# Performance work log

Hardware: AMD Instinct MI355X
Metric: run time of the kernel (lower is better)

The kernel has to match this reference:

```python
import jax, jax.numpy as jnp
import numpy as np

B, C, D = 512, 50000, 256
N_LOADED = 40000


def setup_inputs() -> dict:
    key = jax.random.key(0)
    k1, k2, k3, k4 = jax.random.split(key, 4)
    visual_feats = jax.random.normal(k1, (B, D), dtype=jnp.float32)
    text_feats = jax.random.normal(k2, (C, D), dtype=jnp.float32)
    # sparse multi-hot labels; force class 0 positive for every row so the
    # positive set (intersected with loaded ids) is never empty
    batch_label = (jax.random.uniform(k3, (B, C)) < 0.02).astype(jnp.int32)
    batch_label = batch_label.at[:, 0].set(1)
    # distinct loaded class ids; force id 0 to be loaded
    ids = jax.random.permutation(k4, C)[:N_LOADED].astype(jnp.int32)
    ids = jnp.sort(ids).at[0].set(0)
    return {
        "visual_feats": visual_feats,
        "text_feats": text_feats,
        "batch_label": batch_label,
        "class_ids_loaded": ids,
        "d_space": D,
    }


def reference(visual_feats, text_feats, batch_label, class_ids_loaded, d_space):
    num_classes = text_feats.shape[0]
    # membership mask for loaded class ids (the set() intersection in torch)
    loaded = jnp.zeros((num_classes,), dtype=bool).at[class_ids_loaded].set(True)

    # cosine similarity; note: torch adds 1e-6 eps only to text-feature norms
    v = visual_feats / jnp.linalg.norm(visual_feats, axis=1, keepdims=True)
    t = text_feats / (1e-6 + jnp.linalg.norm(text_feats, axis=1, keepdims=True))
    S = v @ t.T  # [B, C]

    pos = (batch_label != 0) & loaded[None, :]  # ragged positive sets, as mask
    neg = (batch_label == 0) & loaded[None, :]  # ragged negative sets, as mask

    # denominator: sum of exp(sim) over negatives, per row
    denom = jnp.sum(jnp.where(neg, jnp.exp(S), 0.0), axis=1)  # [B]
    n_pos = jnp.sum(pos, axis=1).astype(S.dtype)  # [B]

    # per-row loss: mean over positives of -log(exp(s_p)/denom) = log(denom)-s_p
    per_row = jnp.sum(jnp.where(pos, jnp.log(denom)[:, None] - S, 0.0), axis=1) / n_pos
    return jnp.mean(per_row).reshape(1)
```

## Files before the change

kernel.cpp:

```cpp
#include <hip/hip_runtime.h>
#include <math.h>

#define D_DIM 256
#define TM 128
#define TN 128
#define BK 32
#define NBP 392
#define CBPR 7
#define CBLKS (CBPR * 512)

typedef __attribute__((ext_vector_type(8))) short short8;
typedef __attribute__((ext_vector_type(4))) float floatx4;
typedef unsigned long long u64;

__device__ __forceinline__ unsigned short f2bf(float f) {
    unsigned int u = __float_as_uint(f);
    u += 0x7FFFu + ((u >> 16) & 1u);
    return (unsigned short)(u >> 16);
}

__device__ __forceinline__ void gload16(const void* g, void* lds) {
    __builtin_amdgcn_global_load_lds(
        (const __attribute__((address_space(1))) unsigned int*)g,
        (__attribute__((address_space(3))) unsigned int*)lds, 16, 0, 0);
}

__global__ __launch_bounds__(256) void prep_compress(
    const float* __restrict__ V, const float* __restrict__ T,
    const int* __restrict__ label, const int* __restrict__ ids,
    u64* __restrict__ loadedmask, u64* __restrict__ posmask,
    unsigned short* __restrict__ Vb, unsigned short* __restrict__ Tb,
    float* __restrict__ gaccum, unsigned int* __restrict__ gcount,
    int B, int C, int n_loaded, int WPR) {
    const int bid = blockIdx.x;
    const int tid = threadIdx.x;
    const int lane = tid & 63;

    if (bid < CBLKS) {
        int row = bid / CBPR;
        int sub = bid - row * CBPR;
        int wl  = tid >> 6;
        int w0col = (sub * 4 + wl) * 2048;
        if (w0col >= C) return;
        const int* lp = label + (size_t)row * C;
        int4 lo[4], hi[4];
        #pragma unroll
        for (int r = 0; r < 4; ++r) {
            int c0 = w0col + r * 512 + lane * 8;
            if (c0 < C) {
                lo[r] = *(const int4*)(lp + c0);
                hi[r] = *(const int4*)(lp + c0 + 4);
            } else {
                lo[r] = make_int4(0, 0, 0, 0);
                hi[r] = make_int4(0, 0, 0, 0);
            }
        }
        #pragma unroll
        for (int r = 0; r < 4; ++r) {
            unsigned int by =
                (lo[r].x ? 1u : 0u) | (lo[r].y ? 2u : 0u) |
                (lo[r].z ? 4u : 0u) | (lo[r].w ? 8u : 0u) |
                (hi[r].x ? 16u : 0u) | (hi[r].y ? 32u : 0u) |
                (hi[r].z ? 64u : 0u) | (hi[r].w ? 128u : 0u);
            u64 wv = (u64)by << (8 * (lane & 7));
            wv |= __shfl_xor(wv, 1);
            wv |= __shfl_xor(wv, 2);
            wv |= __shfl_xor(wv, 4);
            if ((lane & 7) == 0) {
                int wc = ((w0col + r * 512) >> 6) + (lane >> 3);
                if (wc < WPR) posmask[(size_t)row * WPR + wc] = wv;
            }
        }
        return;
    }

    int ptid = (bid - CBLKS) * 256 + tid;
    if (ptid == 0) { *gcount = 0u; *gaccum = 0.f; }
    if (ptid < WPR) {
        int base = ptid << 6;
        int lo = 0, hi = n_loaded;
        while (lo < hi) { int mid = (lo + hi) >> 1; if (ids[mid] < base) lo = mid + 1; else hi = mid; }
        u64 m = 0;
        for (int i = lo; i < n_loaded; ++i) {
            int v = ids[i]; if (v >= base + 64) break;
            m |= 1ull << (v - base);
        }
        loadedmask[ptid] = m;
    }
    int wave = ptid >> 6;
    if (wave >= B + C) return;
    bool isV = wave < B;
    const float* src = isV ? (V + (size_t)wave * D_DIM)
                           : (T + (size_t)(wave - B) * D_DIM);
    float4 x = ((const float4*)src)[lane];
    float ss = x.x * x.x + x.y * x.y + x.z * x.z + x.w * x.w;
    #pragma unroll
    for (int off = 32; off > 0; off >>= 1) ss += __shfl_xor(ss, off);
    float nrm = sqrtf(ss);
    float s = isV ? (1.0f / nrm) : (1.0f / (1e-6f + nrm));
    ushort4 o;
    o.x = f2bf(x.x * s); o.y = f2bf(x.y * s);
    o.z = f2bf(x.z * s); o.w = f2bf(x.w * s);
    unsigned short* dst = isV ? (Vb + (size_t)wave * D_DIM)
                              : (Tb + (size_t)(wave - B) * D_DIM);
    ((ushort4*)dst)[lane] = o;
}

__global__ __launch_bounds__(256) void gemm_fused(
    const unsigned short* __restrict__ Vb, const unsigned short* __restrict__ Tb,
    const u64* __restrict__ posmask, const u64* __restrict__ loadedmask,
    float* __restrict__ denomP, float* __restrict__ posP, int C, int WPR) {
    __shared__ unsigned short As[TM * BK];
    __shared__ unsigned short Bs[TN * BK];
    __shared__ float sDen[TM], sPos[TM];

    const int tid  = threadIdx.x;
    const int lane = tid & 63;
    const int w    = tid >> 6;
    const int m0 = blockIdx.x * TM;
    const int n0 = blockIdx.y * TN;

    if (tid < TM) { sDen[tid] = 0.f; sPos[tid] = 0.f; }

    const int sra = lane >> 2;
    const int kc  = (lane & 3) * 8;
    int ga  = m0 + w * 32 + sra;
    int gb0 = n0 + w * 32 + sra;
    int gb1 = gb0 + 16;
    if (gb0 >= C) gb0 = C - 1;
    if (gb1 >= C) gb1 = C - 1;
    const unsigned short* gA0 = Vb + (size_t)ga * D_DIM + kc;
    const unsigned short* gA1 = gA0 + (size_t)16 * D_DIM;
    const unsigned short* gB0 = Tb + (size_t)gb0 * D_DIM + kc;
    const unsigned short* gB1 = Tb + (size_t)gb1 * D_DIM + kc;
    unsigned short* lA0 = &As[w * 32 * BK];
    unsigned short* lA1 = lA0 + 16 * BK;
    unsigned short* lB0 = &Bs[w * 32 * BK];
    unsigned short* lB1 = lB0 + 16 * BK;

    const int wm = (w >> 1) * 64;
    const int wn = (w & 1) * 64;
    const int fr = lane & 15;
    const int quad = lane >> 4;

    floatx4 acc[4][4];
    #pragma unroll
    for (int mi = 0; mi < 4; mi++)
        #pragma unroll
        for (int ni = 0; ni < 4; ni++) acc[mi][ni] = (floatx4)0.f;

    #pragma unroll
    for (int kt = 0; kt < D_DIM / BK; ++kt) {
        if (kt) __syncthreads();
        const int kb = kt * BK;
        gload16(gA0 + kb, lA0);
        gload16(gA1 + kb, lA1);
        gload16(gB0 + kb, lB0);
        gload16(gB1 + kb, lB1);
        __syncthreads();
        short8 af[4], bf[4];
        #pragma unroll
        for (int mi = 0; mi < 4; mi++)
            af[mi] = *(const short8*)&As[(wm + mi * 16 + fr) * BK + quad * 8];
        #pragma unroll
        for (int ni = 0; ni < 4; ni++)
            bf[ni] = *(const short8*)&Bs[(wn + ni * 16 + fr) * BK + quad * 8];
        #pragma unroll
        for (int mi = 0; mi < 4; mi++)
            #pragma unroll
            for (int ni = 0; ni < 4; ni++)
                acc[mi][ni] = __builtin_amdgcn_mfma_f32_16x16x32_bf16(
                    af[mi], bf[ni], acc[mi][ni], 0, 0, 0);
    }

    const int wcol = (n0 + wn) >> 6;
    const u64 loadedw = loadedmask[wcol];
    #pragma unroll
    for (int mi = 0; mi < 4; mi++) {
        #pragma unroll
        for (int i = 0; i < 4; i++) {
            const int mloc = wm + mi * 16 + quad * 4 + i;
            const u64 praw = posmask[(size_t)(m0 + mloc) * WPR + wcol];
            const u64 posw = praw & loadedw;
            const u64 negw = loadedw & ~praw;
            float den = 0.f, pos = 0.f;
            #pragma unroll
            for (int ni = 0; ni < 4; ni++) {
                const float s = acc[mi][ni][i];
                const int bit = ni * 16 + fr;
                if ((negw >> bit) & 1) den += __expf(s);
                if ((posw >> bit) & 1) pos += s;
            }
            #pragma unroll
            for (int off = 8; off >= 1; off >>= 1) {
                den += __shfl_xor(den, off);
                pos += __shfl_xor(pos, off);
            }
            if (fr == 0) {
                if (den != 0.f) atomicAdd(&sDen[mloc], den);
                if (pos != 0.f) atomicAdd(&sPos[mloc], pos);
            }
        }
    }
    __syncthreads();
    if (tid < TM) {
        denomP[(size_t)(m0 + tid) * NBP + blockIdx.y] = sDen[tid];
        posP[(size_t)(m0 + tid) * NBP + blockIdx.y]   = sPos[tid];
    }
}

__global__ void reduce_rows(const float* __restrict__ denomP, const float* __restrict__ posP,
                            const u64* __restrict__ posmask, const u64* __restrict__ loadedmask,
                            float* __restrict__ gaccum, unsigned int* __restrict__ gcount,
                            float* __restrict__ out, int B, int NB, int WPR) {
    __shared__ float bsum[4];
    int wv   = threadIdx.x >> 6;
    int row  = blockIdx.x * 4 + wv;
    int lane = threadIdx.x & 63;
    float den = 0.f, pos = 0.f;
    int cnt = 0;
    if (row < B) {
        for (int bn = lane; bn < NB; bn += 64) {
            den += denomP[(size_t)row * NBP + bn];
            pos += posP[(size_t)row * NBP + bn];
        }
        for (int j = lane; j < WPR; j += 64)
            cnt += __popcll(posmask[(size_t)row * WPR + j] & loadedmask[j]);
        #pragma unroll
        for (int off = 32; off > 0; off >>= 1) {
            den += __shfl_xor(den, off);
            pos += __shfl_xor(pos, off);
            cnt += __shfl_xor(cnt, off);
        }
    }
    if (lane == 0) bsum[wv] = (row < B) ? (logf(den) - pos / (float)cnt) : 0.f;
    __syncthreads();
    if (threadIdx.x == 0) {
        float s = bsum[0] + bsum[1] + bsum[2] + bsum[3];
        atomicAdd(gaccum, s);
        __threadfence();
        unsigned int old = atomicAdd(gcount, 1u);
        if (old == gridDim.x - 1) {
            float tot = atomicAdd(gaccum, 0.0f);
            out[0] = tot / (float)B;
        }
    }
}

extern "C" void kernel_launch(void* const* d_in, const int* in_sizes, int n_in,
                              void* d_out, int out_size, void* d_ws, size_t ws_size,
                              hipStream_t stream) {
    const float* V     = (const float*)d_in[0];
    const float* T     = (const float*)d_in[1];
    const int*   label = (const int*)d_in[2];
    const int*   ids   = (const int*)d_in[3];
    int B = in_sizes[0] / D_DIM;
    int C = in_sizes[1] / D_DIM;
    int n_loaded = in_sizes[3];
    int WPR = (C + 63) >> 6;
    int NB  = (C + TN - 1) / TN;

    char* ws = (char*)d_ws;
    float*        gaccum = (float*)(ws + 0);
    unsigned int* gcount = (unsigned int*)(ws + 8);
    u64*   loadedmask = (u64*)(ws + 2048);
    u64*   posmask    = (u64*)(ws + 8320);
    unsigned short* Vb = (unsigned short*)(ws + 3211392);
    unsigned short* Tb = (unsigned short*)(ws + 3473536);
    float* denomP  = (float*)(ws + 29073536);
    float* posP    = (float*)(ws + 29876352);

    int prep_blocks = ((B + C) * 64 + 255) / 256;
    prep_compress<<<CBLKS + prep_blocks, 256, 0, stream>>>(
        V, T, label, ids, loadedmask, posmask, Vb, Tb, gaccum, gcount,
        B, C, n_loaded, WPR);

    dim3 grid(B / TM, NB);
    gemm_fused<<<grid, 256, 0, stream>>>(Vb, Tb, posmask, loadedmask,
                                         denomP, posP, C, WPR);

    reduce_rows<<<(B + 3) / 4, 256, 0, stream>>>(denomP, posP, posmask, loadedmask,
                                                 gaccum, gcount, (float*)d_out, B, NB, WPR);
}
```

Baseline: 263.3 us.

## Shrink GEMM tiles to 64x64, rework label bit-packing and batch row normalization

The fused GEMM/loss kernel drops from 128x128 to 64x64 tiles, giving about four times as many blocks for the small problem at the cost of less operand reuse per block. The partial-sum buffers and the row reduction are resized to match. Label compression now has each thread read 32 contiguous ints and write one 32-bit mask word, replacing the 8-lane shuffle-based packing. The normalization stage handles two rows per wave to cut launched blocks and overlap loads.

```diff
diff --git a/kernel.cpp b/kernel.cpp
--- a/kernel.cpp
+++ b/kernel.cpp
@@ -2,10 +2,11 @@
 #include <math.h>
 
 #define D_DIM 256
-#define TM 128
-#define TN 128
+#define GTM 64
+#define GTN 64
 #define BK 32
-#define NBP 392
+#define NB 782
+#define NBP 784
 #define CBPR 7
 #define CBLKS (CBPR * 512)
 
@@ -39,37 +40,29 @@
     if (bid < CBLKS) {
         int row = bid / CBPR;
         int sub = bid - row * CBPR;
-        int wl  = tid >> 6;
-        int w0col = (sub * 4 + wl) * 2048;
-        if (w0col >= C) return;
+        int u32idx = sub * 256 + tid;
+        int base = u32idx * 32;
         const int* lp = label + (size_t)row * C;
-        int4 lo[4], hi[4];
-        #pragma unroll
-        for (int r = 0; r < 4; ++r) {
-            int c0 = w0col + r * 512 + lane * 8;
-            if (c0 < C) {
-                lo[r] = *(const int4*)(lp + c0);
-                hi[r] = *(const int4*)(lp + c0 + 4);
-            } else {
-                lo[r] = make_int4(0, 0, 0, 0);
-                hi[r] = make_int4(0, 0, 0, 0);
-            }
-        }
-        #pragma unroll
-        for (int r = 0; r < 4; ++r) {
-            unsigned int by =
-                (lo[r].x ? 1u : 0u) | (lo[r].y ? 2u : 0u) |
-                (lo[r].z ? 4u : 0u) | (lo[r].w ? 8u : 0u) |
-                (hi[r].x ? 16u : 0u) | (hi[r].y ? 32u : 0u) |
-                (hi[r].z ? 64u : 0u) | (hi[r].w ? 128u : 0u);
-            u64 wv = (u64)by << (8 * (lane & 7));
-            wv |= __shfl_xor(wv, 1);
-            wv |= __shfl_xor(wv, 2);
-            wv |= __shfl_xor(wv, 4);
-            if ((lane & 7) == 0) {
-                int wc = ((w0col + r * 512) >> 6) + (lane >> 3);
-                if (wc < WPR) posmask[(size_t)row * WPR + wc] = wv;
-            }
+        unsigned int* prow = (unsigned int*)(posmask + (size_t)row * WPR);
+        if (base + 32 <= C) {
+            int4 q[8];
+            #pragma unroll
+            for (int j = 0; j < 8; ++j) q[j] = *(const int4*)(lp + base + j * 4);
+            unsigned int word = 0;
+            #pragma unroll
+            for (int j = 0; j < 8; ++j) {
+                unsigned int nib = (q[j].x ? 1u : 0u) | (q[j].y ? 2u : 0u) |
+                                   (q[j].z ? 4u : 0u) | (q[j].w ? 8u : 0u);
+                word |= nib << (j * 4);
+            }
+            prow[u32idx] = word;
+        } else if (u32idx < 2 * WPR) {
+            unsigned int word = 0;
+            for (int j = 0; j < 32; ++j) {
+                int col = base + j;
+                if (col < C && lp[col]) word |= 1u << j;
+            }
+            prow[u32idx] = word;
         }
         return;
     }
@@ -87,107 +80,111 @@
         }
         loadedmask[ptid] = m;
     }
-    int wave = ptid >> 6;
-    if (wave >= B + C) return;
-    bool isV = wave < B;
-    const float* src = isV ? (V + (size_t)wave * D_DIM)
-                           : (T + (size_t)(wave - B) * D_DIM);
-    float4 x = ((const float4*)src)[lane];
-    float ss = x.x * x.x + x.y * x.y + x.z * x.z + x.w * x.w;
-    #pragma unroll
-    for (int off = 32; off > 0; off >>= 1) ss += __shfl_xor(ss, off);
-    float nrm = sqrtf(ss);
-    float s = isV ? (1.0f / nrm) : (1.0f / (1e-6f + nrm));
-    ushort4 o;
-    o.x = f2bf(x.x * s); o.y = f2bf(x.y * s);
-    o.z = f2bf(x.z * s); o.w = f2bf(x.w * s);
-    unsigned short* dst = isV ? (Vb + (size_t)wave * D_DIM)
-                              : (Tb + (size_t)(wave - B) * D_DIM);
-    ((ushort4*)dst)[lane] = o;
+    int pwave = (bid - CBLKS) * 4 + (tid >> 6);
+    int r0 = pwave * 2;
+    if (r0 >= B + C) return;
+    float4 x[2];
+    #pragma unroll
+    for (int q = 0; q < 2; ++q) {
+        int wv = r0 + q;
+        if (wv < B + C) {
+            const float* src = (wv < B) ? (V + (size_t)wv * D_DIM)
+                                        : (T + (size_t)(wv - B) * D_DIM);
+            x[q] = ((const float4*)src)[lane];
+        }
+    }
+    #pragma unroll
+    for (int q = 0; q < 2; ++q) {
+        int wv = r0 + q;
+        if (wv >= B + C) break;
+        bool isV = wv < B;
+        float ss = x[q].x * x[q].x + x[q].y * x[q].y + x[q].z * x[q].z + x[q].w * x[q].w;
+        #pragma unroll
+        for (int off = 32; off > 0; off >>= 1) ss += __shfl_xor(ss, off);
+        float nrm = sqrtf(ss);
+        float s = isV ? (1.0f / nrm) : (1.0f / (1e-6f + nrm));
+        ushort4 o;
+        o.x = f2bf(x[q].x * s); o.y = f2bf(x[q].y * s);
+        o.z = f2bf(x[q].z * s); o.w = f2bf(x[q].w * s);
+        unsigned short* dst = isV ? (Vb + (size_t)wv * D_DIM)
+                                  : (Tb + (size_t)(wv - B) * D_DIM);
+        ((ushort4*)dst)[lane] = o;
+    }
 }
 
 __global__ __launch_bounds__(256) void gemm_fused(
     const unsigned short* __restrict__ Vb, const unsigned short* __restrict__ Tb,
     const u64* __restrict__ posmask, const u64* __restrict__ loadedmask,
     float* __restrict__ denomP, float* __restrict__ posP, int C, int WPR) {
-    __shared__ unsigned short As[TM * BK];
-    __shared__ unsigned short Bs[TN * BK];
-    __shared__ float sDen[TM], sPos[TM];
+    __shared__ unsigned short As[GTM * BK];
+    __shared__ unsigned short Bs[GTN * BK];
+    __shared__ float sDen[GTM], sPos[GTM];
 
     const int tid  = threadIdx.x;
     const int lane = tid & 63;
     const int w    = tid >> 6;
-    const int m0 = blockIdx.x * TM;
-    const int n0 = blockIdx.y * TN;
-
-    if (tid < TM) { sDen[tid] = 0.f; sPos[tid] = 0.f; }
+    const int m0 = blockIdx.x * GTM;
+    const int n0 = blockIdx.y * GTN;
+
+    if (tid < GTM) { sDen[tid] = 0.f; sPos[tid] = 0.f; }
 
     const int sra = lane >> 2;
     const int kc  = (lane & 3) * 8;
-    int ga  = m0 + w * 32 + sra;
-    int gb0 = n0 + w * 32 + sra;
-    int gb1 = gb0 + 16;
-    if (gb0 >= C) gb0 = C - 1;
-    if (gb1 >= C) gb1 = C - 1;
-    const unsigned short* gA0 = Vb + (size_t)ga * D_DIM + kc;
-    const unsigned short* gA1 = gA0 + (size_t)16 * D_DIM;
-    const unsigned short* gB0 = Tb + (size_t)gb0 * D_DIM + kc;
-    const unsigned short* gB1 = Tb + (size_t)gb1 * D_DIM + kc;
-    unsigned short* lA0 = &As[w * 32 * BK];
-    unsigned short* lA1 = lA0 + 16 * BK;
-    unsigned short* lB0 = &Bs[w * 32 * BK];
-    unsigned short* lB1 = lB0 + 16 * BK;
-
-    const int wm = (w >> 1) * 64;
-    const int wn = (w & 1) * 64;
+    int ga = m0 + w * 16 + sra;
+    int gb = n0 + w * 16 + sra;
+    if (gb >= C) gb = C - 1;
+    const unsigned short* gA = Vb + (size_t)ga * D_DIM + kc;
+    const unsigned short* gB = Tb + (size_t)gb * D_DIM + kc;
+    unsigned short* lA = &As[w * 16 * BK];
+    unsigned short* lB = &Bs[w * 16 * BK];
+
+    const int wm = (w >> 1) * 32;
+    const int wn = (w & 1) * 32;
     const int fr = lane & 15;
     const int quad = lane >> 4;
 
-    floatx4 acc[4][4];
-    #pragma unroll
-    for (int mi = 0; mi < 4; mi++)
-        #pragma unroll
-        for (int ni = 0; ni < 4; ni++) acc[mi][ni] = (floatx4)0.f;
+    floatx4 acc[2][2];
+    #pragma unroll
+    for (int mi = 0; mi < 2; mi++)
+        #pragma unroll
+        for (int ni = 0; ni < 2; ni++) acc[mi][ni] = (floatx4)0.f;
 
     #pragma unroll
     for (int kt = 0; kt < D_DIM / BK; ++kt) {
         if (kt) __syncthreads();
-        const int kb = kt * BK;
-        gload16(gA0 + kb, lA0);
-        gload16(gA1 + kb, lA1);
-        gload16(gB0 + kb, lB0);
-        gload16(gB1 + kb, lB1);
+        gload16(gA + kt * BK, lA);
+        gload16(gB + kt * BK, lB);
         __syncthreads();
-        short8 af[4], bf[4];
-        #pragma unroll
-        for (int mi = 0; mi < 4; mi++)
+        short8 af[2], bf[2];
+        #pragma unroll
+        for (int mi = 0; mi < 2; mi++)
             af[mi] = *(const short8*)&As[(wm + mi * 16 + fr) * BK + quad * 8];
         #pragma unroll
-        for (int ni = 0; ni < 4; ni++)
+        for (int ni = 0; ni < 2; ni++)
             bf[ni] = *(const short8*)&Bs[(wn + ni * 16 + fr) * BK + quad * 8];
         #pragma unroll
-        for (int mi = 0; mi < 4; mi++)
-            #pragma unroll
-            for (int ni = 0; ni < 4; ni++)
+        for (int mi = 0; mi < 2; mi++)
+            #pragma unroll
+            for (int ni = 0; ni < 2; ni++)
                 acc[mi][ni] = __builtin_amdgcn_mfma_f32_16x16x32_bf16(
                     af[mi], bf[ni], acc[mi][ni], 0, 0, 0);
     }
 
-    const int wcol = (n0 + wn) >> 6;
-    const u64 loadedw = loadedmask[wcol];
-    #pragma unroll
-    for (int mi = 0; mi < 4; mi++) {
+    const int wordIdx = n0 >> 6;
+    const u64 loadedw = loadedmask[wordIdx];
+    #pragma unroll
+    for (int mi = 0; mi < 2; mi++) {
         #pragma unroll
         for (int i = 0; i < 4; i++) {
             const int mloc = wm + mi * 16 + quad * 4 + i;
-            const u64 praw = posmask[(size_t)(m0 + mloc) * WPR + wcol];
+            const u64 praw = posmask[(size_t)(m0 + mloc) * WPR + wordIdx];
             const u64 posw = praw & loadedw;
             const u64 negw = loadedw & ~praw;
             float den = 0.f, pos = 0.f;
             #pragma unroll
-            for (int ni = 0; ni < 4; ni++) {
+            for (int ni = 0; ni < 2; ni++) {
                 const float s = acc[mi][ni][i];
-                const int bit = ni * 16 + fr;
+                const int bit = wn + ni * 16 + fr;
                 if ((negw >> bit) & 1) den += __expf(s);
                 if ((posw >> bit) & 1) pos += s;
             }
@@ -203,7 +200,7 @@
         }
     }
     __syncthreads();
-    if (tid < TM) {
+    if (tid < GTM) {
         denomP[(size_t)(m0 + tid) * NBP + blockIdx.y] = sDen[tid];
         posP[(size_t)(m0 + tid) * NBP + blockIdx.y]   = sPos[tid];
     }
@@ -212,7 +209,7 @@
 __global__ void reduce_rows(const float* __restrict__ denomP, const float* __restrict__ posP,
                             const u64* __restrict__ posmask, const u64* __restrict__ loadedmask,
                             float* __restrict__ gaccum, unsigned int* __restrict__ gcount,
-                            float* __restrict__ out, int B, int NB, int WPR) {
+                            float* __restrict__ out, int B, int WPR) {
     __shared__ float bsum[4];
     int wv   = threadIdx.x >> 6;
     int row  = blockIdx.x * 4 + wv;
@@ -258,7 +255,6 @@
     int C = in_sizes[1] / D_DIM;
     int n_loaded = in_sizes[3];
     int WPR = (C + 63) >> 6;
-    int NB  = (C + TN - 1) / TN;
 
     char* ws = (char*)d_ws;
     float*        gaccum = (float*)(ws + 0);
@@ -268,17 +264,18 @@
     unsigned short* Vb = (unsigned short*)(ws + 3211392);
     unsigned short* Tb = (unsigned short*)(ws + 3473536);
     float* denomP  = (float*)(ws + 29073536);
-    float* posP    = (float*)(ws + 29876352);
-
-    int prep_blocks = ((B + C) * 64 + 255) / 256;
+    float* posP    = (float*)(ws + 30679168);
+
+    int prep_waves  = (B + C + 1) / 2;
+    int prep_blocks = (prep_waves + 3) / 4;
     prep_compress<<<CBLKS + prep_blocks, 256, 0, stream>>>(
         V, T, label, ids, loadedmask, posmask, Vb, Tb, gaccum, gcount,
         B, C, n_loaded, WPR);
 
-    dim3 grid(B / TM, NB);
+    dim3 grid(B / GTM, NB);
     gemm_fused<<<grid, 256, 0, stream>>>(Vb, Tb, posmask, loadedmask,
                                          denomP, posP, C, WPR);
 
     reduce_rows<<<(B + 3) / 4, 256, 0, stream>>>(denomP, posP, posmask, loadedmask,
-                                                 gaccum, gcount, (float*)d_out, B, NB, WPR);
-}
+                                                 gaccum, gcount, (float*)d_out, B, WPR);
+}
```

Result: slower. 269.6 us (+2.4%).
